# Optimization experiments

Measured on AMD Instinct MI355X. Metric: run time of the kernel, lower is better.

Reference implementation:

```python
import jax, jax.numpy as jnp
import numpy as np

GRID_SIZE = 128  # D = H = W
N_POINTS = 8388608


def setup_inputs() -> dict:
    key = jax.random.key(0)
    k_grid, k_coords = jax.random.split(key)
    # occupancy grid buffer: binary {0,1} values as float, shape [D, H, W]
    grid = (jax.random.uniform(k_grid, (GRID_SIZE, GRID_SIZE, GRID_SIZE)) > 0.5).astype(jnp.float32)
    # normalized [-1, 1] query coordinates, layout [..., 3] = (x, y, z)
    coords = jax.random.uniform(k_coords, (N_POINTS, 3), minval=-1.0, maxval=1.0, dtype=jnp.float32)
    return {"grid": grid, "coords": coords}


def _trilinear_sample(grid, coords):
    """torch.nn.functional.grid_sample 5D, mode='bilinear', align_corners=False,
    padding_mode='zeros'. grid: [D,H,W]; coords: [N,3] with (x,y,z) where
    x indexes W, y indexes H, z indexes D. Returns [N]."""
    D, H, W = grid.shape
    x, y, z = coords[:, 0], coords[:, 1], coords[:, 2]
    # unnormalize (align_corners=False): pixel = ((c + 1) * size - 1) / 2
    ix = ((x + 1.0) * W - 1.0) * 0.5
    iy = ((y + 1.0) * H - 1.0) * 0.5
    iz = ((z + 1.0) * D - 1.0) * 0.5

    ix0 = jnp.floor(ix)
    iy0 = jnp.floor(iy)
    iz0 = jnp.floor(iz)
    wx = ix - ix0  # fractional weights
    wy = iy - iy0
    wz = iz - iz0
    ix0 = ix0.astype(jnp.int32)
    iy0 = iy0.astype(jnp.int32)
    iz0 = iz0.astype(jnp.int32)

    def gather(zi, yi, xi):
        # zero padding: out-of-bounds corners contribute 0
        valid = ((zi >= 0) & (zi < D) & (yi >= 0) & (yi < H) & (xi >= 0) & (xi < W))
        zc = jnp.clip(zi, 0, D - 1)
        yc = jnp.clip(yi, 0, H - 1)
        xc = jnp.clip(xi, 0, W - 1)
        return jnp.where(valid, grid[zc, yc, xc], 0.0)

    out = (
        gather(iz0,     iy0,     ix0    ) * (1 - wz) * (1 - wy) * (1 - wx)
        + gather(iz0,     iy0,     ix0 + 1) * (1 - wz) * (1 - wy) * wx
        + gather(iz0,     iy0 + 1, ix0    ) * (1 - wz) * wy       * (1 - wx)
        + gather(iz0,     iy0 + 1, ix0 + 1) * (1 - wz) * wy       * wx
        + gather(iz0 + 1, iy0,     ix0    ) * wz       * (1 - wy) * (1 - wx)
        + gather(iz0 + 1, iy0,     ix0 + 1) * wz       * (1 - wy) * wx
        + gather(iz0 + 1, iy0 + 1, ix0    ) * wz       * wy       * (1 - wx)
        + gather(iz0 + 1, iy0 + 1, ix0 + 1) * wz       * wy       * wx
    )
    return out


def reference(grid, coords):
    flat = coords.reshape(-1, 3)
    return _trilinear_sample(grid, flat)
```

## Files before the change

### kernel.cpp

```cpp
#include <hip/hip_runtime.h>


typedef float fx4 __attribute__((ext_vector_type(4)));

constexpr int GS  = 128;
constexpr int TD  = GS + 1;
constexpr size_t TBL_BYTES  = (size_t)TD * TD * TD;
constexpr size_t MASK_WORDS = (size_t)GS * GS * GS / 64;
constexpr size_t WS_NEEDED  = TBL_BYTES + 8 * MASK_WORDS + 64;

__global__ __launch_bounds__(256)
void bitpack_kernel(const float* __restrict__ grid, unsigned long long* __restrict__ mask) {
    int gid = blockIdx.x * blockDim.x + threadIdx.x;
    float v = __builtin_nontemporal_load(&grid[gid]);
    unsigned long long m = __ballot(v != 0.0f);
    if ((threadIdx.x & 63) == 0) mask[gid >> 6] = m;
}

__device__ __forceinline__ unsigned bit_at(unsigned long long lo, unsigned long long hi, int xi) {
    if ((unsigned)xi >= 128u) return 0u;
    unsigned long long w = (xi < 64) ? lo : hi;
    return (unsigned)((w >> (xi & 63)) & 1ull);
}

__global__ __launch_bounds__(256)
void table_kernel(const unsigned long long* __restrict__ mask, unsigned char* __restrict__ tbl) {
    int i = blockIdx.x * blockDim.x + threadIdx.x;
    if (i >= (int)TBL_BYTES) return;
    int x = i % TD;
    int t = i / TD;
    int y = t % TD;
    int z = t / TD;
    int x0 = x - 1;
    unsigned byte = 0u;
#pragma unroll
    for (int dz = 0; dz < 2; ++dz) {
#pragma unroll
        for (int dy = 0; dy < 2; ++dy) {
            int yi = y - 1 + dy, zi = z - 1 + dz;
            unsigned long long lo = 0ull, hi = 0ull;
            if (((unsigned)yi < 128u) & ((unsigned)zi < 128u)) {
                int r = (zi * 128 + yi) * 2;
                lo = mask[r];
                hi = mask[r + 1];
            }
            unsigned b0 = bit_at(lo, hi, x0);
            unsigned b1 = bit_at(lo, hi, x0 + 1);
            int k = dy * 2 + dz * 4;
            byte |= (b0 << k) | (b1 << (k + 1));
        }
    }
    tbl[i] = (unsigned char)byte;
}

__global__ __launch_bounds__(256)
void sample_packed(const unsigned char* __restrict__ tbl,
                   const float* __restrict__ coords,
                   float* __restrict__ out, int nt) {
    int t = blockIdx.x * blockDim.x + threadIdx.x;
    if (t >= nt) return;
    const fx4* c4 = (const fx4*)coords;
    fx4 q[6];
#pragma unroll
    for (int j = 0; j < 6; ++j) q[j] = __builtin_nontemporal_load(&c4[6 * t + j]);
    const float* f = (const float*)q;

    float wxa[8], wya[8], wza[8];
    int addr[8];
#pragma unroll
    for (int i = 0; i < 8; ++i) {
        float ix = fmaf(f[3 * i + 0], 64.0f, 63.5f);
        float iy = fmaf(f[3 * i + 1], 64.0f, 63.5f);
        float iz = fmaf(f[3 * i + 2], 64.0f, 63.5f);
        float fx = floorf(ix), fy = floorf(iy), fz = floorf(iz);
        wxa[i] = ix - fx; wya[i] = iy - fy; wza[i] = iz - fz;
        int xb = (int)fx + 1, yb = (int)fy + 1, zb = (int)fz + 1;
        xb = min(max(xb, 0), GS); yb = min(max(yb, 0), GS); zb = min(max(zb, 0), GS);
        addr[i] = (zb * TD + yb) * TD + xb;
    }
    unsigned bytes[8];
#pragma unroll
    for (int i = 0; i < 8; ++i) bytes[i] = (unsigned)tbl[addr[i]];
    float o[8];
#pragma unroll
    for (int i = 0; i < 8; ++i) {
        unsigned byte = bytes[i];
        float wx = wxa[i], wy = wya[i], wz = wza[i];
        float v0 = (float)( byte       & 1u);
        float v1 = (float)((byte >> 1) & 1u);
        float v2 = (float)((byte >> 2) & 1u);
        float v3 = (float)((byte >> 3) & 1u);
        float v4 = (float)((byte >> 4) & 1u);
        float v5 = (float)((byte >> 5) & 1u);
        float v6 = (float)((byte >> 6) & 1u);
        float v7 = (float)((byte >> 7) & 1u);
        float c00 = v0 + wx * (v1 - v0);
        float c10 = v2 + wx * (v3 - v2);
        float c01 = v4 + wx * (v5 - v4);
        float c11 = v6 + wx * (v7 - v6);
        float c0  = c00 + wy * (c10 - c00);
        float c1  = c01 + wy * (c11 - c01);
        o[i] = c0 + wz * (c1 - c0);
    }
    fx4* o4 = (fx4*)out;
    fx4 r0 = {o[0], o[1], o[2], o[3]};
    fx4 r1 = {o[4], o[5], o[6], o[7]};
    __builtin_nontemporal_store(r0, &o4[2 * t + 0]);
    __builtin_nontemporal_store(r1, &o4[2 * t + 1]);
}

__global__ __launch_bounds__(256)
void sample_direct(const float* __restrict__ grid,
                   const float* __restrict__ coords,
                   float* __restrict__ out, int nt) {
    int t = blockIdx.x * blockDim.x + threadIdx.x;
    if (t >= nt) return;
    const float4* c4 = (const float4*)coords;
    float4 a = c4[3 * t + 0];
    float4 b = c4[3 * t + 1];
    float4 c = c4[3 * t + 2];
    float xs[4] = {a.x, a.w, b.z, c.y};
    float ys[4] = {a.y, b.x, b.w, c.z};
    float zs[4] = {a.z, b.y, c.x, c.w};
    float4 res;
    float* r = &res.x;
#pragma unroll
    for (int i = 0; i < 4; ++i) {
        float ix = fmaf(xs[i], 64.0f, 63.5f);
        float iy = fmaf(ys[i], 64.0f, 63.5f);
        float iz = fmaf(zs[i], 64.0f, 63.5f);
        float fx = floorf(ix), fy = floorf(iy), fz = floorf(iz);
        float wx = ix - fx, wy = iy - fy, wz = iz - fz;
        int x0 = (int)fx, y0 = (int)fy, z0 = (int)fz;
        float v[8];
#pragma unroll
        for (int k = 0; k < 8; ++k) {
            int xi = x0 + (k & 1);
            int yi = y0 + ((k >> 1) & 1);
            int zi = z0 + (k >> 2);
            bool ok = ((unsigned)xi < (unsigned)GS) &
                      ((unsigned)yi < (unsigned)GS) &
                      ((unsigned)zi < (unsigned)GS);
            int xc = min(max(xi, 0), GS - 1);
            int yc = min(max(yi, 0), GS - 1);
            int zc = min(max(zi, 0), GS - 1);
            v[k] = grid[(zc * GS + yc) * GS + xc] * (ok ? 1.0f : 0.0f);
        }
        float c00 = v[0] + wx * (v[1] - v[0]);
        float c10 = v[2] + wx * (v[3] - v[2]);
        float c01 = v[4] + wx * (v[5] - v[4]);
        float c11 = v[6] + wx * (v[7] - v[6]);
        float c0  = c00 + wy * (c10 - c00);
        float c1  = c01 + wy * (c11 - c01);
        r[i] = c0 + wz * (c1 - c0);
    }
    ((float4*)out)[t] = res;
}

extern "C" void kernel_launch(void* const* d_in, const int* in_sizes, int n_in,
                              void* d_out, int out_size, void* d_ws, size_t ws_size,
                              hipStream_t stream) {
    const float* grid   = (const float*)d_in[0];
    const float* coords = (const float*)d_in[1];
    float* out = (float*)d_out;
    int npts = in_sizes[1] / 3;

    if (ws_size >= WS_NEEDED) {
        unsigned char* tbl = (unsigned char*)d_ws;
        size_t mask_off = (TBL_BYTES + 7) & ~(size_t)7;
        unsigned long long* mask = (unsigned long long*)((char*)d_ws + mask_off);

        int vox = GS * GS * GS;
        bitpack_kernel<<<vox / 256, 256, 0, stream>>>(grid, mask);
        int tbl_blocks = (int)((TBL_BYTES + 255) / 256);
        table_kernel<<<tbl_blocks, 256, 0, stream>>>(mask, tbl);

        int nt = npts / 8;
        sample_packed<<<(nt + 255) / 256, 256, 0, stream>>>(tbl, coords, out, nt);
    } else {
        int nt = npts / 4;
        sample_direct<<<(nt + 255) / 256, 256, 0, stream>>>(grid, coords, out, nt);
    }
}
```

Measured before the change: 212.2 us.

## Sample from LDS-resident bitmask z-slabs instead of a prebuilt corner-byte table

Drops the per-voxel corner-byte table kernel. A new kernel loads half of the bit-packed occupancy mask (about 65 z-planes, roughly 130 KB) into LDS per pass and does the trilinear lookups as LDS word reads plus bit extraction. It uses 1024-thread blocks, each taking a fixed chunk of points, and makes two passes so each point is handled in the pass that owns its z-slab. This avoids building the table and replaces random global/L2 byte gathers with LDS accesses. In exchange, every block reads its coordinates twice, uses scalar scattered output stores, and relies on one large-LDS block per CU plus a point count divisible by the block layout.

```diff
diff --git a/kernel.cpp b/kernel.cpp
--- a/kernel.cpp
+++ b/kernel.cpp
@@ -2,29 +2,112 @@
 
 
 typedef float fx4 __attribute__((ext_vector_type(4)));
-
-constexpr int GS  = 128;
-constexpr int TD  = GS + 1;
+typedef unsigned int u32;
+typedef unsigned long long u64;
+
+constexpr int GS = 128;
+constexpr int TD = GS + 1;
+constexpr size_t MASK_BYTES = (size_t)GS * GS * GS / 8;
 constexpr size_t TBL_BYTES  = (size_t)TD * TD * TD;
-constexpr size_t MASK_WORDS = (size_t)GS * GS * GS / 64;
-constexpr size_t WS_NEEDED  = TBL_BYTES + 8 * MASK_WORDS + 64;
+constexpr size_t WS_NEW = MASK_BYTES;
+constexpr size_t WS_FB  = MASK_BYTES + TBL_BYTES + 64;
+
+constexpr int NP_MAX = 65;
+constexpr size_t SLAB_LDS = (size_t)NP_MAX * 2048 + 16;
 
 __global__ __launch_bounds__(256)
-void bitpack_kernel(const float* __restrict__ grid, unsigned long long* __restrict__ mask) {
+void bitpack_kernel(const float* __restrict__ grid, u64* __restrict__ mask) {
     int gid = blockIdx.x * blockDim.x + threadIdx.x;
-    float v = __builtin_nontemporal_load(&grid[gid]);
-    unsigned long long m = __ballot(v != 0.0f);
+    float v = grid[gid];
+    u64 m = __ballot(v != 0.0f);
     if ((threadIdx.x & 63) == 0) mask[gid >> 6] = m;
 }
 
-__device__ __forceinline__ unsigned bit_at(unsigned long long lo, unsigned long long hi, int xi) {
+__global__ __launch_bounds__(1024, 4)
+void sample_slab(const u32* __restrict__ mask32,
+                 const float* __restrict__ coords,
+                 float* __restrict__ out, int npts) {
+    extern __shared__ u32 lds[];
+    const int tid = threadIdx.x;
+    const int nthr = 1024;
+    const int ptsPerBlock = npts / gridDim.x;
+    const int base = blockIdx.x * ptsPerBlock;
+    const int ngroups = ptsPerBlock / (4 * nthr);
+    const fx4* c4 = (const fx4*)coords;
+
+#pragma unroll 1
+    for (int s = 0; s < 2; ++s) {
+        const int pz0 = s ? 63 : 0;
+        const int np  = s ? 65 : 64;
+        const int zlo = s ? 64 : 0;
+        const int zhi = s ? 128 : 63;
+        __syncthreads();
+        {
+            const int nwords = np * 512;
+            const u32* src = mask32 + pz0 * 512;
+            for (int i = tid; i < nwords; i += nthr) lds[i] = src[i];
+            if (tid == 0) lds[nwords] = 0;
+        }
+        __syncthreads();
+
+        for (int g = 0; g < ngroups; ++g) {
+            int grp = base / 4 + g * nthr + tid;
+            fx4 q0 = c4[3 * grp + 0];
+            fx4 q1 = c4[3 * grp + 1];
+            fx4 q2 = c4[3 * grp + 2];
+            float f[12] = {q0.x, q0.y, q0.z, q0.w,
+                           q1.x, q1.y, q1.z, q1.w,
+                           q2.x, q2.y, q2.z, q2.w};
+#pragma unroll
+            for (int j = 0; j < 4; ++j) {
+                float ixf = fmaf(f[3 * j + 0], 64.0f, 63.5f);
+                float iyf = fmaf(f[3 * j + 1], 64.0f, 63.5f);
+                float izf = fmaf(f[3 * j + 2], 64.0f, 63.5f);
+                float fxx = floorf(ixf), fyy = floorf(iyf), fzz = floorf(izf);
+                float wx = ixf - fxx, wy = iyf - fyy, wz = izf - fzz;
+                int x0 = (int)fxx, y0 = (int)fyy, z0 = (int)fzz;
+                int zb = z0 + 1;
+                if (zb >= zlo && zb <= zhi) {
+                    int xc = x0 < 0 ? 0 : x0;
+                    int k  = xc >> 5;
+                    int p0 = x0 - (k << 5);
+                    u32 okx0 = (u32)(x0 >= 0);
+                    u32 okx1 = (u32)(x0 <= 126);
+                    float r[2][2];
+#pragma unroll
+                    for (int dz = 0; dz < 2; ++dz) {
+                        int zl = z0 + dz - pz0;
+                        u32 vz = (u32)((unsigned)zl < (unsigned)np);
+#pragma unroll
+                        for (int dy = 0; dy < 2; ++dy) {
+                            int yr = y0 + dy;
+                            u32 v = vz & (u32)((unsigned)yr < 128u);
+                            int widx = v ? (zl * 128 + yr) * 4 + k : 0;
+                            u32 w0 = lds[widx];
+                            u32 w1 = lds[widx + 1];
+                            u64 vv = (u64)w0 | ((u64)w1 << 32);
+                            int b0 = (int)((u32)(vv >> (p0 & 63)) & 1u & okx0 & v);
+                            int b1 = (int)((u32)(vv >> ((p0 + 1) & 63)) & 1u & okx1 & v);
+                            r[dz][dy] = fmaf(wx, (float)(b1 - b0), (float)b0);
+                        }
+                    }
+                    float c0 = fmaf(wy, r[0][1] - r[0][0], r[0][0]);
+                    float c1 = fmaf(wy, r[1][1] - r[1][0], r[1][0]);
+                    out[grp * 4 + j] = fmaf(wz, c1 - c0, c0);
+                }
+            }
+        }
+    }
+}
+
+__device__ __forceinline__ unsigned bit_at(u64 lo, u64 hi, int xi) {
     if ((unsigned)xi >= 128u) return 0u;
-    unsigned long long w = (xi < 64) ? lo : hi;
+    u64 w = (xi < 64) ? lo : hi;
     return (unsigned)((w >> (xi & 63)) & 1ull);
 }
 
 __global__ __launch_bounds__(256)
-void table_kernel(const unsigned long long* __restrict__ mask, unsigned char* __restrict__ tbl) {
+void table_kernel(const u64* __restrict__ mask, unsigned char* __restrict__ tbl) {
     int i = blockIdx.x * blockDim.x + threadIdx.x;
     if (i >= (int)TBL_BYTES) return;
     int x = i % TD;
@@ -38,16 +121,14 @@
 #pragma unroll
         for (int dy = 0; dy < 2; ++dy) {
             int yi = y - 1 + dy, zi = z - 1 + dz;
-            unsigned long long lo = 0ull, hi = 0ull;
+            u64 lo = 0ull, hi = 0ull;
             if (((unsigned)yi < 128u) & ((unsigned)zi < 128u)) {
                 int r = (zi * 128 + yi) * 2;
                 lo = mask[r];
                 hi = mask[r + 1];
             }
-            unsigned b0 = bit_at(lo, hi, x0);
-            unsigned b1 = bit_at(lo, hi, x0 + 1);
-            int k = dy * 2 + dz * 4;
-            byte |= (b0 << k) | (b1 << (k + 1));
+            int kk = dy * 2 + dz * 4;
+            byte |= (bit_at(lo, hi, x0) << kk) | (bit_at(lo, hi, x0 + 1) << (kk + 1));
         }
     }
     tbl[i] = (unsigned char)byte;
@@ -62,9 +143,8 @@
     const fx4* c4 = (const fx4*)coords;
     fx4 q[6];
 #pragma unroll
-    for (int j = 0; j < 6; ++j) q[j] = __builtin_nontemporal_load(&c4[6 * t + j]);
+    for (int j = 0; j < 6; ++j) q[j] = c4[6 * t + j];
     const float* f = (const float*)q;
-
     float wxa[8], wya[8], wza[8];
     int addr[8];
 #pragma unroll
@@ -75,7 +155,6 @@
         float fx = floorf(ix), fy = floorf(iy), fz = floorf(iz);
         wxa[i] = ix - fx; wya[i] = iy - fy; wza[i] = iz - fz;
         int xb = (int)fx + 1, yb = (int)fy + 1, zb = (int)fz + 1;
-        xb = min(max(xb, 0), GS); yb = min(max(yb, 0), GS); zb = min(max(zb, 0), GS);
         addr[i] = (zb * TD + yb) * TD + xb;
     }
     unsigned bytes[8];
@@ -105,56 +184,8 @@
     fx4* o4 = (fx4*)out;
     fx4 r0 = {o[0], o[1], o[2], o[3]};
     fx4 r1 = {o[4], o[5], o[6], o[7]};
-    __builtin_nontemporal_store(r0, &o4[2 * t + 0]);
-    __builtin_nontemporal_store(r1, &o4[2 * t + 1]);
-}
-
-__global__ __launch_bounds__(256)
-void sample_direct(const float* __restrict__ grid,
-                   const float* __restrict__ coords,
-                   float* __restrict__ out, int nt) {
-    int t = blockIdx.x * blockDim.x + threadIdx.x;
-    if (t >= nt) return;
-    const float4* c4 = (const float4*)coords;
-    float4 a = c4[3 * t + 0];
-    float4 b = c4[3 * t + 1];
-    float4 c = c4[3 * t + 2];
-    float xs[4] = {a.x, a.w, b.z, c.y};
-    float ys[4] = {a.y, b.x, b.w, c.z};
-    float zs[4] = {a.z, b.y, c.x, c.w};
-    float4 res;
-    float* r = &res.x;
-#pragma unroll
-    for (int i = 0; i < 4; ++i) {
-        float ix = fmaf(xs[i], 64.0f, 63.5f);
-        float iy = fmaf(ys[i], 64.0f, 63.5f);
-        float iz = fmaf(zs[i], 64.0f, 63.5f);
-        float fx = floorf(ix), fy = floorf(iy), fz = floorf(iz);
-        float wx = ix - fx, wy = iy - fy, wz = iz - fz;
-        int x0 = (int)fx, y0 = (int)fy, z0 = (int)fz;
-        float v[8];
-#pragma unroll
-        for (int k = 0; k < 8; ++k) {
-            int xi = x0 + (k & 1);
-            int yi = y0 + ((k >> 1) & 1);
-            int zi = z0 + (k >> 2);
-            bool ok = ((unsigned)xi < (unsigned)GS) &
-                      ((unsigned)yi < (unsigned)GS) &
-                      ((unsigned)zi < (unsigned)GS);
-            int xc = min(max(xi, 0), GS - 1);
-            int yc = min(max(yi, 0), GS - 1);
-            int zc = min(max(zi, 0), GS - 1);
-            v[k] = grid[(zc * GS + yc) * GS + xc] * (ok ? 1.0f : 0.0f);
-        }
-        float c00 = v[0] + wx * (v[1] - v[0]);
-        float c10 = v[2] + wx * (v[3] - v[2]);
-        float c01 = v[4] + wx * (v[5] - v[4]);
-        float c11 = v[6] + wx * (v[7] - v[6]);
-        float c0  = c00 + wy * (c10 - c00);
-        float c1  = c01 + wy * (c11 - c01);
-        r[i] = c0 + wz * (c1 - c0);
-    }
-    ((float4*)out)[t] = res;
+    o4[2 * t + 0] = r0;
+    o4[2 * t + 1] = r1;
 }
 
 extern "C" void kernel_launch(void* const* d_in, const int* in_sizes, int n_in,
@@ -165,20 +196,27 @@
     float* out = (float*)d_out;
     int npts = in_sizes[1] / 3;
 
-    if (ws_size >= WS_NEEDED) {
-        unsigned char* tbl = (unsigned char*)d_ws;
-        size_t mask_off = (TBL_BYTES + 7) & ~(size_t)7;
-        unsigned long long* mask = (unsigned long long*)((char*)d_ws + mask_off);
-
-        int vox = GS * GS * GS;
+    u64* mask = (u64*)d_ws;
+    int vox = GS * GS * GS;
+
+    (void)hipFuncSetAttribute((const void*)sample_slab,
+                              hipFuncAttributeMaxDynamicSharedMemorySize,
+                              (int)SLAB_LDS);
+    int nb = 0;
+    hipError_t oe = hipOccupancyMaxActiveBlocksPerMultiprocessor(
+        &nb, sample_slab, 1024, SLAB_LDS);
+    bool slab_ok = (oe == hipSuccess) && (nb >= 1) && (ws_size >= WS_NEW) &&
+                   (npts % (256 * 4096) == 0);
+
+    if (slab_ok) {
+        bitpack_kernel<<<vox / 256, 256, 0, stream>>>(grid, mask);
+        sample_slab<<<256, 1024, SLAB_LDS, stream>>>((const u32*)mask, coords, out, npts);
+    } else if (ws_size >= WS_FB) {
+        unsigned char* tbl = (unsigned char*)d_ws + MASK_BYTES;
         bitpack_kernel<<<vox / 256, 256, 0, stream>>>(grid, mask);
         int tbl_blocks = (int)((TBL_BYTES + 255) / 256);
         table_kernel<<<tbl_blocks, 256, 0, stream>>>(mask, tbl);
-
         int nt = npts / 8;
         sample_packed<<<(nt + 255) / 256, 256, 0, stream>>>(tbl, coords, out, nt);
-    } else {
-        int nt = npts / 4;
-        sample_direct<<<(nt + 255) / 256, 256, 0, stream>>>(grid, coords, out, nt);
-    }
-}
+    }
+}
```

After: 201.5 us. -5.0%, faster.
